# Kernel optimization log

Measured on AMD Instinct MI355X. Metric: run time of the kernel, lower is better.

## Reference

```python
import jax, jax.numpy as jnp
import numpy as np

S, M, H, E = 8192, 1024, 4096, 8
CAPACITY = S // E  # capacity_factor = 1.0, k = 1


def setup_inputs() -> dict:
    key = jax.random.key(0)
    ks = jax.random.split(key, 4)
    return {
        "x": jax.random.normal(ks[0], (S, M), jnp.float32),
        "wg": jax.random.normal(ks[1], (M, E), jnp.float32) * 0.02,
        "inter_w": jax.random.normal(ks[2], (E, M, H), jnp.float32) * 0.02,
        "inter_b": jnp.zeros((E, H), jnp.float32),
        "output_w": jax.random.normal(ks[3], (E, H, M), jnp.float32) * 0.02,
        "output_b": jnp.zeros((E, M), jnp.float32),
    }


def _top1_gate(x, wg, capacity):
    """GShard-style top-1 gate (inference: no noise, drop tokens over capacity).
    Returns combine_weights [S,E,C] (float) and dispatch_mask [S,E,C] (float 0/1)."""
    logits = x @ wg                                   # [S,E]
    gates = jax.nn.softmax(logits, axis=-1)           # [S,E]
    idx = jnp.argmax(gates, axis=-1)                  # [S]
    mask1 = jax.nn.one_hot(idx, gates.shape[-1], dtype=gates.dtype)  # [S,E]
    # 0-based position of each token within its expert's queue
    locations = jnp.cumsum(mask1, axis=0) - mask1     # [S,E]
    mask1 = mask1 * (locations < capacity)            # drop overflow tokens
    pos = jnp.sum(locations * mask1, axis=1).astype(jnp.int32)  # [S]
    gate_s = jnp.sum(gates * mask1, axis=1)           # [S] gate value of kept tokens
    loc_oh = jax.nn.one_hot(pos, capacity, dtype=gates.dtype)    # [S,C]
    combine = gate_s[:, None, None] * mask1[:, :, None] * loc_oh[:, None, :]  # [S,E,C]
    dispatch = (combine > 0).astype(x.dtype)
    return combine, dispatch


def reference(x, wg, inter_w, inter_b, output_w, output_b):
    combine, dispatch = _top1_gate(x, wg, CAPACITY)
    # token dispatch: torch.einsum('sec,sm->ecm', dispatch_mask, attention_output)
    disp_x = jnp.einsum('sec,sm->ecm', dispatch, x)                 # [E,C,M]
    # per-expert fused gelu-GEMM MLP (gelu_gemm_func: gelu(x@W1+b1)@W2, +b2)
    h = jax.nn.gelu(jnp.einsum('ecm,emh->ech', disp_x, inter_w)
                    + inter_b[:, None, :], approximate=False)       # [E,C,H]
    exp_out = jnp.einsum('ech,ehm->ecm', h, output_w) + output_b[:, None, :]  # [E,C,M]
    # combine: combined_weights.reshape(S, E*C) @ expert_output.reshape(E*C, M)
    y = jnp.einsum('sec,ecm->sm', combine, exp_out)                 # [S,M]
    return y
```

## Files before the change

kernel.cpp:

```cpp
#include <hip/hip_runtime.h>

#define S_ 8192
#define M_ 1024
#define H_ 4096
#define E_ 8
#define C_ 1024

typedef short s16x8 __attribute__((ext_vector_type(8)));
typedef float f32x4 __attribute__((ext_vector_type(4)));

__device__ inline unsigned short f2bf(float f) {
    unsigned int u = __float_as_uint(f);
    unsigned int r = u + 0x7fffu + ((u >> 16) & 1u);
    return (unsigned short)(r >> 16);
}

union Frag8 { s16x8 v; unsigned short s[8]; };

__global__ __launch_bounds__(256) void gate_kernel(
    const float* __restrict__ x, const float* __restrict__ wg,
    int* __restrict__ expert_of, float* __restrict__ gate_full)
{
    int token = (blockIdx.x * 256 + threadIdx.x) >> 6;
    int lane  = threadIdx.x & 63;
    const float* xr = x + (size_t)token * M_;
    double acc[E_] = {0,0,0,0,0,0,0,0};
    for (int t = 0; t < M_ / 64; ++t) {
        int m = t * 64 + lane;
        double xv = (double)xr[m];
        const float* w = wg + m * E_;
        #pragma unroll
        for (int e = 0; e < E_; ++e) acc[e] += xv * (double)w[e];
    }
    #pragma unroll
    for (int e = 0; e < E_; ++e)
        for (int off = 32; off; off >>= 1) acc[e] += __shfl_xor(acc[e], off);
    if (lane == 0) {
        double mx = acc[0]; int idx = 0;
        #pragma unroll
        for (int e = 1; e < E_; ++e) if (acc[e] > mx) { mx = acc[e]; idx = e; }
        double den = 0.0;
        #pragma unroll
        for (int e = 0; e < E_; ++e) den += exp(acc[e] - mx);
        expert_of[token] = idx;
        gate_full[token] = (float)(1.0 / den);
    }
}

__global__ __launch_bounds__(256) void scan_kernel(
    const int* __restrict__ expert_of, int* __restrict__ slot_to_token)
{
    __shared__ int wave_cnt[4][E_];
    __shared__ int base_[E_];
    int tid = threadIdx.x, lane = tid & 63, wv = tid >> 6;
    for (int i = tid; i < E_ * C_; i += 256) slot_to_token[i] = -1;
    if (tid < E_) base_[tid] = 0;
    __syncthreads();
    for (int chunk = 0; chunk < S_ / 256; ++chunk) {
        int s = chunk * 256 + tid;
        int e = expert_of[s];
        unsigned long long mymask = 0;
        #pragma unroll
        for (int j = 0; j < E_; ++j) {
            unsigned long long b = __ballot(e == j);
            if (lane == 0) wave_cnt[wv][j] = __popcll(b);
            if (j == e) mymask = b;
        }
        __syncthreads();
        int wave_off = 0;
        for (int w2 = 0; w2 < wv; ++w2) wave_off += wave_cnt[w2][e];
        int pos = base_[e] + wave_off +
                  __popcll(mymask & ((1ull << lane) - 1ull));
        __syncthreads();
        if (tid < E_) {
            int hsum = 0;
            #pragma unroll
            for (int w2 = 0; w2 < 4; ++w2) hsum += wave_cnt[w2][tid];
            base_[tid] += hsum;
        }
        if (pos < C_) slot_to_token[e * C_ + pos] = s;
        __syncthreads();
    }
}

__global__ __launch_bounds__(256) void gemm1_kernel(
    const float* __restrict__ x, const float* __restrict__ w1,
    const float* __restrict__ b1, const int* __restrict__ slot_to_token,
    unsigned short* __restrict__ h, int e_base)
{
    const int e    = e_base + blockIdx.z;
    const int eloc = blockIdx.z;
    const int n0 = blockIdx.x * 128;
    const int c0 = blockIdx.y * 128;
    const float* B = w1 + (size_t)e * M_ * H_;

    __shared__ unsigned short As[128 * 40];
    __shared__ unsigned short Bs[128 * 36];
    __shared__ int tok[128];

    int tid = threadIdx.x;
    if (tid < 128) tok[tid] = slot_to_token[e * C_ + c0 + tid];
    __syncthreads();

    f32x4 acc[4][4] = {};
    int lane = tid & 63;
    int wv = tid >> 6, wr = wv >> 1, wc = wv & 1;
    int qd = lane >> 4, ln16 = lane & 15;

    for (int k0 = 0; k0 < M_; k0 += 32) {
        #pragma unroll
        for (int v = 0; v < 4; ++v) {
            int idx = v * 256 + tid;
            int r = idx >> 3, ks = (idx & 7) * 4;
            float4 val;
            int t = tok[r];
            if (t >= 0) val = *(const float4*)(x + (size_t)t * M_ + k0 + ks);
            else        val = make_float4(0.f, 0.f, 0.f, 0.f);
            unsigned short* dst = &As[r * 40 + ks];
            unsigned long long packed =
                (unsigned long long)f2bf(val.x)
              | ((unsigned long long)f2bf(val.y) << 16)
              | ((unsigned long long)f2bf(val.z) << 32)
              | ((unsigned long long)f2bf(val.w) << 48);
            *(unsigned long long*)dst = packed;
        }
        {
            int n = tid & 127;
            int kb = (tid >> 7) * 4;
            #pragma unroll
            for (int v = 0; v < 4; ++v) {
                int k4 = kb + v * 8;
                float a0 = B[(size_t)(k0 + k4 + 0) * H_ + n0 + n];
                float a1 = B[(size_t)(k0 + k4 + 1) * H_ + n0 + n];
                float a2 = B[(size_t)(k0 + k4 + 2) * H_ + n0 + n];
                float a3 = B[(size_t)(k0 + k4 + 3) * H_ + n0 + n];
                unsigned long long packed =
                    (unsigned long long)f2bf(a0)
                  | ((unsigned long long)f2bf(a1) << 16)
                  | ((unsigned long long)f2bf(a2) << 32)
                  | ((unsigned long long)f2bf(a3) << 48);
                *(unsigned long long*)(&Bs[n * 36 + k4]) = packed;
            }
        }
        __syncthreads();

        s16x8 af[4], bfr[4];
        #pragma unroll
        for (int i = 0; i < 4; ++i) {
            int m = wr * 64 + i * 16 + ln16;
            af[i] = *(const s16x8*)(&As[m * 40 + qd * 8]);
        }
        #pragma unroll
        for (int j = 0; j < 4; ++j) {
            int n = wc * 64 + j * 16 + ln16;
            unsigned long long lo = *(const unsigned long long*)(&Bs[n * 36 + qd * 8]);
            unsigned long long hi = *(const unsigned long long*)(&Bs[n * 36 + qd * 8 + 4]);
            Frag8 f;
            *(unsigned long long*)(&f.s[0]) = lo;
            *(unsigned long long*)(&f.s[4]) = hi;
            bfr[j] = f.v;
        }
        #pragma unroll
        for (int i = 0; i < 4; ++i)
            #pragma unroll
            for (int j = 0; j < 4; ++j)
                acc[i][j] = __builtin_amdgcn_mfma_f32_16x16x32_bf16(
                    af[i], bfr[j], acc[i][j], 0, 0, 0);
        __syncthreads();
    }

    unsigned short* hb = h + (size_t)eloc * C_ * H_;
    #pragma unroll
    for (int i = 0; i < 4; ++i) {
        #pragma unroll
        for (int j = 0; j < 4; ++j) {
            int n = n0 + wc * 64 + j * 16 + ln16;
            float bias = b1[e * H_ + n];
            #pragma unroll
            for (int r = 0; r < 4; ++r) {
                int c = c0 + wr * 64 + i * 16 + qd * 4 + r;
                float v = acc[i][j][r] + bias;
                float g = 0.5f * v * (1.0f + erff(v * 0.70710678118f));
                hb[(size_t)c * H_ + n] = f2bf(g);
            }
        }
    }
}

__global__ __launch_bounds__(256) void gemm2_kernel(
    const unsigned short* __restrict__ h, const float* __restrict__ w2,
    const float* __restrict__ b2, const int* __restrict__ slot_to_token,
    const float* __restrict__ gate_full, float* __restrict__ y, int e_base)
{
    const int e    = e_base + blockIdx.z;
    const int eloc = blockIdx.z;
    const int n0 = blockIdx.x * 128;
    const int c0 = blockIdx.y * 128;
    const unsigned short* A = h + (size_t)eloc * C_ * H_;
    const float* B = w2 + (size_t)e * H_ * M_;

    __shared__ unsigned short As[128 * 40];
    __shared__ unsigned short Bs[128 * 36];
    __shared__ int tok[128];

    int tid = threadIdx.x;
    if (tid < 128) tok[tid] = slot_to_token[e * C_ + c0 + tid];
    __syncthreads();

    f32x4 acc[4][4] = {};
    int lane = tid & 63;
    int wv = tid >> 6, wr = wv >> 1, wc = wv & 1;
    int qd = lane >> 4, ln16 = lane & 15;

    for (int k0 = 0; k0 < H_; k0 += 32) {
        #pragma unroll
        for (int v = 0; v < 2; ++v) {
            int idx = v * 256 + tid;
            int r = idx >> 2, q = idx & 3;
            *(uint4*)(&As[r * 40 + q * 8]) =
                *(const uint4*)(A + (size_t)(c0 + r) * H_ + k0 + q * 8);
        }
        {
            int n = tid & 127;
            int kb = (tid >> 7) * 4;
            #pragma unroll
            for (int v = 0; v < 4; ++v) {
                int k4 = kb + v * 8;
                float a0 = B[(size_t)(k0 + k4 + 0) * M_ + n0 + n];
                float a1 = B[(size_t)(k0 + k4 + 1) * M_ + n0 + n];
                float a2 = B[(size_t)(k0 + k4 + 2) * M_ + n0 + n];
                float a3 = B[(size_t)(k0 + k4 + 3) * M_ + n0 + n];
                unsigned long long packed =
                    (unsigned long long)f2bf(a0)
                  | ((unsigned long long)f2bf(a1) << 16)
                  | ((unsigned long long)f2bf(a2) << 32)
                  | ((unsigned long long)f2bf(a3) << 48);
                *(unsigned long long*)(&Bs[n * 36 + k4]) = packed;
            }
        }
        __syncthreads();

        s16x8 af[4], bfr[4];
        #pragma unroll
        for (int i = 0; i < 4; ++i) {
            int m = wr * 64 + i * 16 + ln16;
            af[i] = *(const s16x8*)(&As[m * 40 + qd * 8]);
        }
        #pragma unroll
        for (int j = 0; j < 4; ++j) {
            int n = wc * 64 + j * 16 + ln16;
            unsigned long long lo = *(const unsigned long long*)(&Bs[n * 36 + qd * 8]);
            unsigned long long hi = *(const unsigned long long*)(&Bs[n * 36 + qd * 8 + 4]);
            Frag8 f;
            *(unsigned long long*)(&f.s[0]) = lo;
            *(unsigned long long*)(&f.s[4]) = hi;
            bfr[j] = f.v;
        }
        #pragma unroll
        for (int i = 0; i < 4; ++i)
            #pragma unroll
            for (int j = 0; j < 4; ++j)
                acc[i][j] = __builtin_amdgcn_mfma_f32_16x16x32_bf16(
                    af[i], bfr[j], acc[i][j], 0, 0, 0);
        __syncthreads();
    }

    #pragma unroll
    for (int i = 0; i < 4; ++i) {
        #pragma unroll
        for (int r = 0; r < 4; ++r) {
            int c = wr * 64 + i * 16 + qd * 4 + r;
            int t = tok[c];
            if (t < 0) continue;
            float g = gate_full[t];
            float* yr = y + (size_t)t * M_;
            #pragma unroll
            for (int j = 0; j < 4; ++j) {
                int n = n0 + wc * 64 + j * 16 + ln16;
                yr[n] = g * (acc[i][j][r] + b2[e * M_ + n]);
            }
        }
    }
}

extern "C" void kernel_launch(void* const* d_in, const int* in_sizes, int n_in,
                              void* d_out, int out_size, void* d_ws, size_t ws_size,
                              hipStream_t stream) {
    const float* x  = (const float*)d_in[0];
    const float* wg = (const float*)d_in[1];
    const float* w1 = (const float*)d_in[2];
    const float* b1 = (const float*)d_in[3];
    const float* w2 = (const float*)d_in[4];
    const float* b2 = (const float*)d_in[5];
    float* y = (float*)d_out;

    char* ws = (char*)d_ws;
    int*   expert_of     = (int*)ws;
    int*   slot_to_token = (int*)(ws + 32768);
    float* gate_full     = (float*)(ws + 65536);
    unsigned short* h    = (unsigned short*)(ws + 98304);

    size_t h_avail = (ws_size > 98304) ? ws_size - 98304 : 0;
    int ec = (int)(h_avail / ((size_t)C_ * H_ * 2));
    if (ec < 1) ec = 1;
    if (ec > E_) ec = E_;

    hipMemsetAsync(d_out, 0, (size_t)S_ * M_ * sizeof(float), stream);
    gate_kernel<<<S_ / 4, 256, 0, stream>>>(x, wg, expert_of, gate_full);
    scan_kernel<<<1, 256, 0, stream>>>(expert_of, slot_to_token);
    for (int e0 = 0; e0 < E_; e0 += ec) {
        int cnt = (E_ - e0 < ec) ? (E_ - e0) : ec;
        gemm1_kernel<<<dim3(H_ / 128, C_ / 128, cnt), 256, 0, stream>>>(
            x, w1, b1, slot_to_token, h, e0);
        gemm2_kernel<<<dim3(M_ / 128, C_ / 128, cnt), 256, 0, stream>>>(
            h, w2, b2, slot_to_token, gate_full, y, e0);
    }
}
```

Before: 711.0 us.

## Pre-convert activations and weights to bf16 K-major and stream GEMM tiles directly into LDS

The gate kernel now also writes a bf16 copy of x. A new transpose-convert kernel turns each expert's fp32 weights into K-major bf16 before each GEMM. Both GEMMs then fill their LDS tiles with 16-byte global_load_lds direct-to-LDS copies, replacing the per-iteration fp32 loads, bf16 conversion and scalar strided weight reads. The cost is extra passes over the full weight tensors on every call and a larger workspace. Removing the LDS row padding may introduce bank conflicts on fragment reads.

```diff
diff --git a/kernel.cpp b/kernel.cpp
--- a/kernel.cpp
+++ b/kernel.cpp
@@ -9,25 +9,33 @@
 typedef short s16x8 __attribute__((ext_vector_type(8)));
 typedef float f32x4 __attribute__((ext_vector_type(4)));
 
-__device__ inline unsigned short f2bf(float f) {
+__device__ __forceinline__ unsigned short f2bf(float f) {
     unsigned int u = __float_as_uint(f);
     unsigned int r = u + 0x7fffu + ((u >> 16) & 1u);
     return (unsigned short)(r >> 16);
 }
 
-union Frag8 { s16x8 v; unsigned short s[8]; };
+__device__ __forceinline__ void async_copy16(const unsigned short* g, unsigned short* l) {
+    __builtin_amdgcn_global_load_lds(
+        (const __attribute__((address_space(1))) unsigned int*)g,
+        (__attribute__((address_space(3))) unsigned int*)l, 16, 0, 0);
+}
 
 __global__ __launch_bounds__(256) void gate_kernel(
     const float* __restrict__ x, const float* __restrict__ wg,
-    int* __restrict__ expert_of, float* __restrict__ gate_full)
+    int* __restrict__ expert_of, float* __restrict__ gate_full,
+    unsigned short* __restrict__ xb)
 {
     int token = (blockIdx.x * 256 + threadIdx.x) >> 6;
     int lane  = threadIdx.x & 63;
     const float* xr = x + (size_t)token * M_;
+    unsigned short* xbr = xb + (size_t)token * M_;
     double acc[E_] = {0,0,0,0,0,0,0,0};
     for (int t = 0; t < M_ / 64; ++t) {
         int m = t * 64 + lane;
-        double xv = (double)xr[m];
+        float xf = xr[m];
+        xbr[m] = f2bf(xf);
+        double xv = (double)xf;
         const float* w = wg + m * E_;
         #pragma unroll
         for (int e = 0; e < E_; ++e) acc[e] += xv * (double)w[e];
@@ -83,82 +91,103 @@
     }
 }
 
+__global__ __launch_bounds__(256) void transpose_cvt_kernel(
+    const float* __restrict__ src, unsigned short* __restrict__ dst,
+    int K, int N, int e_base)
+{
+    __shared__ unsigned short tile[64 * 84];
+    const size_t esz = (size_t)K * N;
+    const float* s = src + (size_t)(e_base + blockIdx.z) * esz;
+    unsigned short* d = dst + (size_t)blockIdx.z * esz;
+    const int k0 = blockIdx.y * 64, n0 = blockIdx.x * 64;
+    const int tid = threadIdx.x;
+    {
+        const int n  = tid & 63;
+        const int kb = (tid >> 6) * 16;
+        #pragma unroll
+        for (int i = 0; i < 4; ++i) {
+            int k4 = kb + i * 4;
+            float a0 = s[(size_t)(k0 + k4 + 0) * N + n0 + n];
+            float a1 = s[(size_t)(k0 + k4 + 1) * N + n0 + n];
+            float a2 = s[(size_t)(k0 + k4 + 2) * N + n0 + n];
+            float a3 = s[(size_t)(k0 + k4 + 3) * N + n0 + n];
+            unsigned long long p = (unsigned long long)f2bf(a0)
+                | ((unsigned long long)f2bf(a1) << 16)
+                | ((unsigned long long)f2bf(a2) << 32)
+                | ((unsigned long long)f2bf(a3) << 48);
+            *(unsigned long long*)(&tile[n * 84 + k4]) = p;
+        }
+    }
+    __syncthreads();
+    {
+        const int n  = tid >> 3;
+        const int k8 = (tid & 7) * 8;
+        #pragma unroll
+        for (int j = 0; j < 2; ++j) {
+            int nn = n + j * 32;
+            unsigned long long lo = *(const unsigned long long*)(&tile[nn * 84 + k8]);
+            unsigned long long hi = *(const unsigned long long*)(&tile[nn * 84 + k8 + 4]);
+            ulonglong2 v; v.x = lo; v.y = hi;
+            *(ulonglong2*)(d + (size_t)(n0 + nn) * K + k0 + k8) = v;
+        }
+    }
+}
+
 __global__ __launch_bounds__(256) void gemm1_kernel(
-    const float* __restrict__ x, const float* __restrict__ w1,
+    const unsigned short* __restrict__ xb, const unsigned short* __restrict__ w1t,
     const float* __restrict__ b1, const int* __restrict__ slot_to_token,
     unsigned short* __restrict__ h, int e_base)
 {
-    const int e    = e_base + blockIdx.z;
     const int eloc = blockIdx.z;
+    const int e    = e_base + eloc;
     const int n0 = blockIdx.x * 128;
     const int c0 = blockIdx.y * 128;
-    const float* B = w1 + (size_t)e * M_ * H_;
-
-    __shared__ unsigned short As[128 * 40];
-    __shared__ unsigned short Bs[128 * 36];
+
+    __shared__ unsigned short As[128 * 32];
+    __shared__ unsigned short Bs[128 * 32];
     __shared__ int tok[128];
 
-    int tid = threadIdx.x;
+    const int tid = threadIdx.x;
     if (tid < 128) tok[tid] = slot_to_token[e * C_ + c0 + tid];
     __syncthreads();
 
+    const int q0 = tid, q1 = 256 + tid;
+    const int r0 = q0 >> 2, cq0 = q0 & 3;
+    const int r1 = q1 >> 2, cq1 = q1 & 3;
+    int t0 = tok[r0]; if (t0 < 0) t0 = 0;
+    int t1 = tok[r1]; if (t1 < 0) t1 = 0;
+    const unsigned short* srcA0 = xb + (size_t)t0 * M_ + cq0 * 8;
+    const unsigned short* srcA1 = xb + (size_t)t1 * M_ + cq1 * 8;
+    const unsigned short* Bp = w1t + (size_t)eloc * M_ * H_;
+    const unsigned short* srcB0 = Bp + (size_t)(n0 + r0) * M_ + cq0 * 8;
+    const unsigned short* srcB1 = Bp + (size_t)(n0 + r1) * M_ + cq1 * 8;
+    const int wave = tid >> 6;
+    unsigned short* dstA0 = As + wave * 512;
+    unsigned short* dstA1 = As + 2048 + wave * 512;
+    unsigned short* dstB0 = Bs + wave * 512;
+    unsigned short* dstB1 = Bs + 2048 + wave * 512;
+
     f32x4 acc[4][4] = {};
-    int lane = tid & 63;
-    int wv = tid >> 6, wr = wv >> 1, wc = wv & 1;
-    int qd = lane >> 4, ln16 = lane & 15;
+    const int lane = tid & 63;
+    const int wr = wave >> 1, wc = wave & 1;
+    const int qd = lane >> 4, ln16 = lane & 15;
 
     for (int k0 = 0; k0 < M_; k0 += 32) {
-        #pragma unroll
-        for (int v = 0; v < 4; ++v) {
-            int idx = v * 256 + tid;
-            int r = idx >> 3, ks = (idx & 7) * 4;
-            float4 val;
-            int t = tok[r];
-            if (t >= 0) val = *(const float4*)(x + (size_t)t * M_ + k0 + ks);
-            else        val = make_float4(0.f, 0.f, 0.f, 0.f);
-            unsigned short* dst = &As[r * 40 + ks];
-            unsigned long long packed =
-                (unsigned long long)f2bf(val.x)
-              | ((unsigned long long)f2bf(val.y) << 16)
-              | ((unsigned long long)f2bf(val.z) << 32)
-              | ((unsigned long long)f2bf(val.w) << 48);
-            *(unsigned long long*)dst = packed;
-        }
-        {
-            int n = tid & 127;
-            int kb = (tid >> 7) * 4;
-            #pragma unroll
-            for (int v = 0; v < 4; ++v) {
-                int k4 = kb + v * 8;
-                float a0 = B[(size_t)(k0 + k4 + 0) * H_ + n0 + n];
-                float a1 = B[(size_t)(k0 + k4 + 1) * H_ + n0 + n];
-                float a2 = B[(size_t)(k0 + k4 + 2) * H_ + n0 + n];
-                float a3 = B[(size_t)(k0 + k4 + 3) * H_ + n0 + n];
-                unsigned long long packed =
-                    (unsigned long long)f2bf(a0)
-                  | ((unsigned long long)f2bf(a1) << 16)
-                  | ((unsigned long long)f2bf(a2) << 32)
-                  | ((unsigned long long)f2bf(a3) << 48);
-                *(unsigned long long*)(&Bs[n * 36 + k4]) = packed;
-            }
-        }
-        __syncthreads();
-
+        async_copy16(srcA0 + k0, dstA0);
+        async_copy16(srcA1 + k0, dstA1);
+        async_copy16(srcB0 + k0, dstB0);
+        async_copy16(srcB1 + k0, dstB1);
+        __syncthreads();
         s16x8 af[4], bfr[4];
         #pragma unroll
         for (int i = 0; i < 4; ++i) {
             int m = wr * 64 + i * 16 + ln16;
-            af[i] = *(const s16x8*)(&As[m * 40 + qd * 8]);
+            af[i] = *(const s16x8*)(&As[m * 32 + qd * 8]);
         }
         #pragma unroll
         for (int j = 0; j < 4; ++j) {
             int n = wc * 64 + j * 16 + ln16;
-            unsigned long long lo = *(const unsigned long long*)(&Bs[n * 36 + qd * 8]);
-            unsigned long long hi = *(const unsigned long long*)(&Bs[n * 36 + qd * 8 + 4]);
-            Frag8 f;
-            *(unsigned long long*)(&f.s[0]) = lo;
-            *(unsigned long long*)(&f.s[4]) = hi;
-            bfr[j] = f.v;
+            bfr[j] = *(const s16x8*)(&Bs[n * 32 + qd * 8]);
         }
         #pragma unroll
         for (int i = 0; i < 4; ++i)
@@ -188,73 +217,59 @@
 }
 
 __global__ __launch_bounds__(256) void gemm2_kernel(
-    const unsigned short* __restrict__ h, const float* __restrict__ w2,
+    const unsigned short* __restrict__ h, const unsigned short* __restrict__ w2t,
     const float* __restrict__ b2, const int* __restrict__ slot_to_token,
     const float* __restrict__ gate_full, float* __restrict__ y, int e_base)
 {
-    const int e    = e_base + blockIdx.z;
     const int eloc = blockIdx.z;
+    const int e    = e_base + eloc;
     const int n0 = blockIdx.x * 128;
     const int c0 = blockIdx.y * 128;
-    const unsigned short* A = h + (size_t)eloc * C_ * H_;
-    const float* B = w2 + (size_t)e * H_ * M_;
-
-    __shared__ unsigned short As[128 * 40];
-    __shared__ unsigned short Bs[128 * 36];
+
+    __shared__ unsigned short As[128 * 32];
+    __shared__ unsigned short Bs[128 * 32];
     __shared__ int tok[128];
 
-    int tid = threadIdx.x;
+    const int tid = threadIdx.x;
     if (tid < 128) tok[tid] = slot_to_token[e * C_ + c0 + tid];
     __syncthreads();
 
+    const int q0 = tid, q1 = 256 + tid;
+    const int r0 = q0 >> 2, cq0 = q0 & 3;
+    const int r1 = q1 >> 2, cq1 = q1 & 3;
+    const unsigned short* Ap = h + (size_t)eloc * C_ * H_;
+    const unsigned short* srcA0 = Ap + (size_t)(c0 + r0) * H_ + cq0 * 8;
+    const unsigned short* srcA1 = Ap + (size_t)(c0 + r1) * H_ + cq1 * 8;
+    const unsigned short* Bp = w2t + (size_t)eloc * H_ * M_;
+    const unsigned short* srcB0 = Bp + (size_t)(n0 + r0) * H_ + cq0 * 8;
+    const unsigned short* srcB1 = Bp + (size_t)(n0 + r1) * H_ + cq1 * 8;
+    const int wave = tid >> 6;
+    unsigned short* dstA0 = As + wave * 512;
+    unsigned short* dstA1 = As + 2048 + wave * 512;
+    unsigned short* dstB0 = Bs + wave * 512;
+    unsigned short* dstB1 = Bs + 2048 + wave * 512;
+
     f32x4 acc[4][4] = {};
-    int lane = tid & 63;
-    int wv = tid >> 6, wr = wv >> 1, wc = wv & 1;
-    int qd = lane >> 4, ln16 = lane & 15;
+    const int lane = tid & 63;
+    const int wr = wave >> 1, wc = wave & 1;
+    const int qd = lane >> 4, ln16 = lane & 15;
 
     for (int k0 = 0; k0 < H_; k0 += 32) {
-        #pragma unroll
-        for (int v = 0; v < 2; ++v) {
-            int idx = v * 256 + tid;
-            int r = idx >> 2, q = idx & 3;
-            *(uint4*)(&As[r * 40 + q * 8]) =
-                *(const uint4*)(A + (size_t)(c0 + r) * H_ + k0 + q * 8);
-        }
-        {
-            int n = tid & 127;
-            int kb = (tid >> 7) * 4;
-            #pragma unroll
-            for (int v = 0; v < 4; ++v) {
-                int k4 = kb + v * 8;
-                float a0 = B[(size_t)(k0 + k4 + 0) * M_ + n0 + n];
-                float a1 = B[(size_t)(k0 + k4 + 1) * M_ + n0 + n];
-                float a2 = B[(size_t)(k0 + k4 + 2) * M_ + n0 + n];
-                float a3 = B[(size_t)(k0 + k4 + 3) * M_ + n0 + n];
-                unsigned long long packed =
-                    (unsigned long long)f2bf(a0)
-                  | ((unsigned long long)f2bf(a1) << 16)
-                  | ((unsigned long long)f2bf(a2) << 32)
-                  | ((unsigned long long)f2bf(a3) << 48);
-                *(unsigned long long*)(&Bs[n * 36 + k4]) = packed;
-            }
-        }
-        __syncthreads();
-
+        async_copy16(srcA0 + k0, dstA0);
+        async_copy16(srcA1 + k0, dstA1);
+        async_copy16(srcB0 + k0, dstB0);
+        async_copy16(srcB1 + k0, dstB1);
+        __syncthreads();
         s16x8 af[4], bfr[4];
         #pragma unroll
         for (int i = 0; i < 4; ++i) {
             int m = wr * 64 + i * 16 + ln16;
-            af[i] = *(const s16x8*)(&As[m * 40 + qd * 8]);
+            af[i] = *(const s16x8*)(&As[m * 32 + qd * 8]);
         }
         #pragma unroll
         for (int j = 0; j < 4; ++j) {
             int n = wc * 64 + j * 16 + ln16;
-            unsigned long long lo = *(const unsigned long long*)(&Bs[n * 36 + qd * 8]);
-            unsigned long long hi = *(const unsigned long long*)(&Bs[n * 36 + qd * 8 + 4]);
-            Frag8 f;
-            *(unsigned long long*)(&f.s[0]) = lo;
-            *(unsigned long long*)(&f.s[4]) = hi;
-            bfr[j] = f.v;
+            bfr[j] = *(const s16x8*)(&Bs[n * 32 + qd * 8]);
         }
         #pragma unroll
         for (int i = 0; i < 4; ++i)
@@ -298,21 +313,33 @@
     int*   expert_of     = (int*)ws;
     int*   slot_to_token = (int*)(ws + 32768);
     float* gate_full     = (float*)(ws + 65536);
-    unsigned short* h    = (unsigned short*)(ws + 98304);
-
-    size_t h_avail = (ws_size > 98304) ? ws_size - 98304 : 0;
-    int ec = (int)(h_avail / ((size_t)C_ * H_ * 2));
+    unsigned short* xb   = (unsigned short*)(ws + 98304);
+
+    const size_t xb_bytes = (size_t)S_ * M_ * 2;
+    const size_t per_e    = (size_t)M_ * H_ * 2;
+    size_t base = 98304 + xb_bytes;
+    size_t avail = (ws_size > base) ? ws_size - base : 0;
+    int ec = (int)(avail / (3 * per_e));
     if (ec < 1) ec = 1;
     if (ec > E_) ec = E_;
 
+    unsigned short* h   = (unsigned short*)(ws + base);
+    unsigned short* w1t = h   + (size_t)ec * C_ * H_;
+    unsigned short* w2t = w1t + (size_t)ec * M_ * H_;
+
     hipMemsetAsync(d_out, 0, (size_t)S_ * M_ * sizeof(float), stream);
-    gate_kernel<<<S_ / 4, 256, 0, stream>>>(x, wg, expert_of, gate_full);
+    gate_kernel<<<S_ / 4, 256, 0, stream>>>(x, wg, expert_of, gate_full, xb);
     scan_kernel<<<1, 256, 0, stream>>>(expert_of, slot_to_token);
+
     for (int e0 = 0; e0 < E_; e0 += ec) {
         int cnt = (E_ - e0 < ec) ? (E_ - e0) : ec;
+        transpose_cvt_kernel<<<dim3(H_ / 64, M_ / 64, cnt), 256, 0, stream>>>(
+            w1, w1t, M_, H_, e0);
         gemm1_kernel<<<dim3(H_ / 128, C_ / 128, cnt), 256, 0, stream>>>(
-            x, w1, b1, slot_to_token, h, e0);
+            xb, w1t, b1, slot_to_token, h, e0);
+        transpose_cvt_kernel<<<dim3(M_ / 64, H_ / 64, cnt), 256, 0, stream>>>(
+            w2, w2t, H_, M_, e0);
         gemm2_kernel<<<dim3(M_ / 128, C_ / 128, cnt), 256, 0, stream>>>(
-            h, w2, b2, slot_to_token, gate_full, y, e0);
-    }
-}
+            h, w2t, b2, slot_to_token, gate_full, y, e0);
+    }
+}
```

Measured after the change: 602.8 us. -15.2%, faster.
